# Optimization experiments

Hardware: AMD Instinct MI355X
Metric: run time of the kernel (lower is better)

## Reference

```python
import jax, jax.numpy as jnp
import numpy as np


def setup_inputs() -> dict:
    key = jax.random.key(0)
    k1, k2 = jax.random.split(key)
    B, T, D, K = 16, 800, 256, 64
    x = jax.random.normal(k1, (B, T, D), dtype=jnp.float32)
    mu = jax.random.normal(k2, (K, D), dtype=jnp.float32)
    prec = jnp.ones((K,), dtype=jnp.float32)
    return {"x": x, "mu": mu, "prec": prec}


def reference(x, mu, prec):
    # x: (B,T,D), mu: (K,D), prec: (K,)
    delta = x[:, :, None, :] - mu[None, None, :, :]          # (B,T,K,D)
    dist = jnp.sum(delta * delta, axis=-1)                   # (B,T,K) dist_pow=2
    llk = -(prec * prec) * dist                              # use_bias=False -> bias=0
    r = jax.nn.softmax(llk, axis=-1)                         # softmax over components K
    r = r / (jnp.sum(r, axis=1, keepdims=True) + 1e-9)       # normalize over time T
    pool = jnp.einsum('btk,btkd->bkd', r, delta)             # weighted sum over T
    return pool.reshape(x.shape[0], -1)                      # (B, K*D)
```

## Files before the change

kernel.cpp:

```cpp
#include <hip/hip_runtime.h>

#define B_ 16
#define T_ 800
#define D_ 256
#define K_ 64
#define NTILE 13
#define TSPLIT 8

__global__ __launch_bounds__(512, 1) void kernelA(
    const float* __restrict__ x, const float* __restrict__ mu,
    const float* __restrict__ prec, float* __restrict__ r2, float* __restrict__ Spart)
{
    __shared__ float xs[64 * 260];
    __shared__ float mus[64 * 260];
    __shared__ float xxs[64];
    __shared__ float mms[64];
    __shared__ float sred[8][64];

    const int tid  = threadIdx.x;
    const int tx   = tid >> 4;
    const int ky   = tid & 15;
    const int b    = blockIdx.x / NTILE;
    const int tile = blockIdx.x % NTILE;
    const int t0   = tile * 64;

    #pragma unroll
    for (int jj = 0; jj < 8; ++jj) {
        const int g   = tid + jj * 512;
        const int row = g >> 6, col = g & 63;
        int trow = t0 + row; if (trow > T_ - 1) trow = T_ - 1;
        *(float4*)&xs[row * 260 + col * 4] =
            *(const float4*)(x + ((size_t)(b * T_ + trow)) * D_ + col * 4);
        *(float4*)&mus[row * 260 + col * 4] =
            *(const float4*)(mu + (size_t)row * D_ + col * 4);
    }
    __syncthreads();

    {
        const int srow = tid >> 3, sq = tid & 7;
        float xxp = 0.f, mmp = 0.f;
        #pragma unroll
        for (int m = 0; m < 8; ++m) {
            float4 v = *(const float4*)&xs[srow * 260 + (sq * 8 + m) * 4];
            xxp = fmaf(v.x, v.x, xxp); xxp = fmaf(v.y, v.y, xxp);
            xxp = fmaf(v.z, v.z, xxp); xxp = fmaf(v.w, v.w, xxp);
            float4 u = *(const float4*)&mus[srow * 260 + (sq * 8 + m) * 4];
            mmp = fmaf(u.x, u.x, mmp); mmp = fmaf(u.y, u.y, mmp);
            mmp = fmaf(u.z, u.z, mmp); mmp = fmaf(u.w, u.w, mmp);
        }
        xxp += __shfl_xor(xxp, 1); xxp += __shfl_xor(xxp, 2); xxp += __shfl_xor(xxp, 4);
        mmp += __shfl_xor(mmp, 1); mmp += __shfl_xor(mmp, 2); mmp += __shfl_xor(mmp, 4);
        if (sq == 0) { xxs[srow] = xxp; mms[srow] = mmp; }
    }
    __syncthreads();

    float acc[2][4];
    #pragma unroll
    for (int i = 0; i < 2; ++i)
        #pragma unroll
        for (int j = 0; j < 4; ++j) acc[i][j] = 0.f;

    #pragma unroll 4
    for (int dg = 0; dg < 64; ++dg) {
        float4 xv[2], mv[4];
        #pragma unroll
        for (int i = 0; i < 2; ++i) xv[i] = *(const float4*)&xs[(tx * 2 + i) * 260 + dg * 4];
        #pragma unroll
        for (int j = 0; j < 4; ++j) mv[j] = *(const float4*)&mus[(ky + 16 * j) * 260 + dg * 4];
        #pragma unroll
        for (int i = 0; i < 2; ++i)
            #pragma unroll
            for (int j = 0; j < 4; ++j) {
                float a = acc[i][j];
                a = fmaf(xv[i].x, mv[j].x, a);
                a = fmaf(xv[i].y, mv[j].y, a);
                a = fmaf(xv[i].z, mv[j].z, a);
                a = fmaf(xv[i].w, mv[j].w, a);
                acc[i][j] = a;
            }
    }

    float p2[4], mmk[4];
    #pragma unroll
    for (int j = 0; j < 4; ++j) {
        float p = prec[ky + 16 * j];
        p2[j] = p * p;
        mmk[j] = mms[ky + 16 * j];
    }

    float sacc[4] = {0.f, 0.f, 0.f, 0.f};
    #pragma unroll
    for (int i = 0; i < 2; ++i) {
        const int tl = tx * 2 + i;
        const bool valid = (t0 + tl) < T_;
        const float xxv = xxs[tl];
        float llk[4];
        #pragma unroll
        for (int j = 0; j < 4; ++j)
            llk[j] = p2[j] * (2.f * acc[i][j] - xxv - mmk[j]);
        float mx = fmaxf(fmaxf(llk[0], llk[1]), fmaxf(llk[2], llk[3]));
        mx = fmaxf(mx, __shfl_xor(mx, 1)); mx = fmaxf(mx, __shfl_xor(mx, 2));
        mx = fmaxf(mx, __shfl_xor(mx, 4)); mx = fmaxf(mx, __shfl_xor(mx, 8));
        float e[4], ps = 0.f;
        #pragma unroll
        for (int j = 0; j < 4; ++j) { e[j] = __expf(llk[j] - mx); ps += e[j]; }
        ps += __shfl_xor(ps, 1); ps += __shfl_xor(ps, 2);
        ps += __shfl_xor(ps, 4); ps += __shfl_xor(ps, 8);
        const float inv = 1.f / ps;
        float4 rv;
        rv.x = e[0] * inv; rv.y = e[1] * inv; rv.z = e[2] * inv; rv.w = e[3] * inv;
        if (valid) {
            *(float4*)(r2 + (size_t)(b * T_ + t0 + tl) * K_ + ky * 4) = rv;
            sacc[0] += rv.x; sacc[1] += rv.y; sacc[2] += rv.z; sacc[3] += rv.w;
        }
    }

    #pragma unroll
    for (int j = 0; j < 4; ++j) {
        sacc[j] += __shfl_xor(sacc[j], 16);
        sacc[j] += __shfl_xor(sacc[j], 32);
    }
    const int w = tid >> 6;
    if ((tid & 48) == 0) {
        #pragma unroll
        for (int j = 0; j < 4; ++j) sred[w][ky * 4 + j] = sacc[j];
    }
    __syncthreads();
    if (tid < 64) {
        const int k = tid;
        const int slot = (k & 15) * 4 + (k >> 4);
        float s = 0.f;
        #pragma unroll
        for (int q = 0; q < 8; ++q) s += sred[q][slot];
        Spart[((size_t)b * NTILE + tile) * K_ + k] = s;
    }
}

__global__ __launch_bounds__(256, 2) void kernelB(
    const float* __restrict__ x, const float* __restrict__ r2, float* __restrict__ Pp)
{
    __shared__ float xs[50 * 68];
    __shared__ float rs[50 * 68];

    const int tid = threadIdx.x;
    const int kx  = tid >> 4;
    const int dy  = tid & 15;
    const int bid = blockIdx.x;
    const int b   = bid >> 5;
    const int dc  = (bid >> 3) & 3;
    const int ts  = bid & 7;

    float4 acc[4];
    #pragma unroll
    for (int j = 0; j < 4; ++j) acc[j] = make_float4(0.f, 0.f, 0.f, 0.f);

    #pragma unroll 1
    for (int sc = 0; sc < 2; ++sc) {
        const int tbase = ts * 100 + sc * 50;
        __syncthreads();
        #pragma unroll
        for (int jj = 0; jj < 4; ++jj) {
            const int idx = tid + jj * 256;
            if (idx < 800) {
                const int row = idx >> 4, f4i = idx & 15;
                *(float4*)&xs[row * 68 + f4i * 4] =
                    *(const float4*)(x + (size_t)(b * T_ + tbase + row) * D_ + dc * 64 + f4i * 4);
                *(float4*)&rs[row * 68 + f4i * 4] =
                    *(const float4*)(r2 + (size_t)(b * T_ + tbase + row) * K_ + f4i * 4);
            }
        }
        __syncthreads();
        #pragma unroll 5
        for (int tt = 0; tt < 50; ++tt) {
            const float4 rv = *(const float4*)&rs[tt * 68 + kx * 4];
            const float4 xv = *(const float4*)&xs[tt * 68 + dy * 4];
            acc[0].x = fmaf(rv.x, xv.x, acc[0].x); acc[0].y = fmaf(rv.x, xv.y, acc[0].y);
            acc[0].z = fmaf(rv.x, xv.z, acc[0].z); acc[0].w = fmaf(rv.x, xv.w, acc[0].w);
            acc[1].x = fmaf(rv.y, xv.x, acc[1].x); acc[1].y = fmaf(rv.y, xv.y, acc[1].y);
            acc[1].z = fmaf(rv.y, xv.z, acc[1].z); acc[1].w = fmaf(rv.y, xv.w, acc[1].w);
            acc[2].x = fmaf(rv.z, xv.x, acc[2].x); acc[2].y = fmaf(rv.z, xv.y, acc[2].y);
            acc[2].z = fmaf(rv.z, xv.z, acc[2].z); acc[2].w = fmaf(rv.z, xv.w, acc[2].w);
            acc[3].x = fmaf(rv.w, xv.x, acc[3].x); acc[3].y = fmaf(rv.w, xv.y, acc[3].y);
            acc[3].z = fmaf(rv.w, xv.z, acc[3].z); acc[3].w = fmaf(rv.w, xv.w, acc[3].w);
        }
    }

    #pragma unroll
    for (int j = 0; j < 4; ++j) {
        const int k = kx + 16 * j;
        *(float4*)(Pp + (((size_t)ts * B_ + b) * K_ + k) * D_ + dc * 64 + dy * 4) = acc[j];
    }
}

__global__ __launch_bounds__(256) void kernelC(
    const float* __restrict__ Pp, const float* __restrict__ Spart,
    const float* __restrict__ mu, float* __restrict__ out)
{
    const int o4 = blockIdx.x * 256 + threadIdx.x;
    const int d4 = o4 & 63;
    const int k  = (o4 >> 6) & 63;
    const int b  = o4 >> 12;

    float s = 0.f;
    #pragma unroll
    for (int p = 0; p < NTILE; ++p)
        s += Spart[((size_t)b * NTILE + p) * K_ + k];

    float4 acc = make_float4(0.f, 0.f, 0.f, 0.f);
    #pragma unroll
    for (int ts = 0; ts < TSPLIT; ++ts) {
        float4 v = ((const float4*)Pp)[(((size_t)ts * B_ + b) * K_ + k) * 64 + d4];
        acc.x += v.x; acc.y += v.y; acc.z += v.z; acc.w += v.w;
    }
    const float inv = 1.f / (s + 1e-9f);
    const float sm  = s * inv;
    float4 m = ((const float4*)mu)[k * 64 + d4];
    float4 o;
    o.x = acc.x * inv - sm * m.x;
    o.y = acc.y * inv - sm * m.y;
    o.z = acc.z * inv - sm * m.z;
    o.w = acc.w * inv - sm * m.w;
    ((float4*)out)[o4] = o;
}

extern "C" void kernel_launch(void* const* d_in, const int* in_sizes, int n_in,
                              void* d_out, int out_size, void* d_ws, size_t ws_size,
                              hipStream_t stream) {
    const float* x    = (const float*)d_in[0];
    const float* mu   = (const float*)d_in[1];
    const float* prec = (const float*)d_in[2];
    float* out = (float*)d_out;

    float* r2    = (float*)d_ws;
    float* Pp    = r2 + (size_t)B_ * T_ * K_;
    float* Spart = Pp + (size_t)TSPLIT * B_ * K_ * D_;

    kernelA<<<B_ * NTILE, 512, 0, stream>>>(x, mu, prec, r2, Spart);
    kernelB<<<B_ * 4 * TSPLIT, 256, 0, stream>>>(x, r2, Pp);
    kernelC<<<256, 256, 0, stream>>>(Pp, Spart, mu, out);
}
```

Measured before the change: 88.93 us.

## Fuse responsibility-weighted pooling into distance kernel with atomic accumulation

Merges the softmax kernel and the pooling GEMM kernel into one. Responsibilities are kept in shared memory and multiplied against the x tile already resident in LDS, so the r2 write/read round trip through global memory and one kernel launch go away. Partial pooled sums from the 13 time tiles are combined with float atomicAdd into a zeroed buffer, which replaces the TSPLIT partial buffer and its reduction in kernelC. The cost is a memset, heavy atomic traffic (13 blocks contending per output element), a longer kernelA with extra LDS use, and nondeterministic summation order.

```diff
diff --git a/kernel.cpp b/kernel.cpp
--- a/kernel.cpp
+++ b/kernel.cpp
@@ -5,14 +5,14 @@
 #define D_ 256
 #define K_ 64
 #define NTILE 13
-#define TSPLIT 8
-
-__global__ __launch_bounds__(512, 1) void kernelA(
+
+__global__ __launch_bounds__(512, 1) void kernelAB(
     const float* __restrict__ x, const float* __restrict__ mu,
-    const float* __restrict__ prec, float* __restrict__ r2, float* __restrict__ Spart)
+    const float* __restrict__ prec, float* __restrict__ P, float* __restrict__ Spart)
 {
     __shared__ float xs[64 * 260];
     __shared__ float mus[64 * 260];
+    __shared__ float rt[64 * 68];
     __shared__ float xxs[64];
     __shared__ float mms[64];
     __shared__ float sred[8][64];
@@ -106,13 +106,11 @@
         for (int j = 0; j < 4; ++j) { e[j] = __expf(llk[j] - mx); ps += e[j]; }
         ps += __shfl_xor(ps, 1); ps += __shfl_xor(ps, 2);
         ps += __shfl_xor(ps, 4); ps += __shfl_xor(ps, 8);
-        const float inv = 1.f / ps;
+        const float inv = valid ? (1.f / ps) : 0.f;
         float4 rv;
         rv.x = e[0] * inv; rv.y = e[1] * inv; rv.z = e[2] * inv; rv.w = e[3] * inv;
-        if (valid) {
-            *(float4*)(r2 + (size_t)(b * T_ + t0 + tl) * K_ + ky * 4) = rv;
-            sacc[0] += rv.x; sacc[1] += rv.y; sacc[2] += rv.z; sacc[3] += rv.w;
-        }
+        *(float4*)&rt[tl * 68 + ky * 4] = rv;
+        sacc[0] += rv.x; sacc[1] += rv.y; sacc[2] += rv.z; sacc[3] += rv.w;
     }
 
     #pragma unroll
@@ -134,66 +132,54 @@
         for (int q = 0; q < 8; ++q) s += sred[q][slot];
         Spart[((size_t)b * NTILE + tile) * K_ + k] = s;
     }
+
+    const int dhalf = tid & 31;
+    const int kx2   = tid >> 5;
+
+    float4 pa[4][2];
+    #pragma unroll
+    for (int j = 0; j < 4; ++j) {
+        pa[j][0] = make_float4(0.f, 0.f, 0.f, 0.f);
+        pa[j][1] = make_float4(0.f, 0.f, 0.f, 0.f);
+    }
+
+    #pragma unroll 8
+    for (int tt = 0; tt < 64; ++tt) {
+        const float4 rv  = *(const float4*)&rt[tt * 68 + kx2 * 4];
+        const float4 xv0 = *(const float4*)&xs[tt * 260 + dhalf * 4];
+        const float4 xv1 = *(const float4*)&xs[tt * 260 + 128 + dhalf * 4];
+        #pragma unroll
+        for (int j = 0; j < 4; ++j) {
+            const float rj = (j == 0) ? rv.x : (j == 1) ? rv.y : (j == 2) ? rv.z : rv.w;
+            pa[j][0].x = fmaf(rj, xv0.x, pa[j][0].x);
+            pa[j][0].y = fmaf(rj, xv0.y, pa[j][0].y);
+            pa[j][0].z = fmaf(rj, xv0.z, pa[j][0].z);
+            pa[j][0].w = fmaf(rj, xv0.w, pa[j][0].w);
+            pa[j][1].x = fmaf(rj, xv1.x, pa[j][1].x);
+            pa[j][1].y = fmaf(rj, xv1.y, pa[j][1].y);
+            pa[j][1].z = fmaf(rj, xv1.z, pa[j][1].z);
+            pa[j][1].w = fmaf(rj, xv1.w, pa[j][1].w);
+        }
+    }
+
+    float* Pb = P + (size_t)b * K_ * D_;
+    #pragma unroll
+    for (int j = 0; j < 4; ++j) {
+        const int k = kx2 + 16 * j;
+        float* dst = Pb + (size_t)k * D_ + dhalf * 4;
+        atomicAdd(dst + 0, pa[j][0].x);
+        atomicAdd(dst + 1, pa[j][0].y);
+        atomicAdd(dst + 2, pa[j][0].z);
+        atomicAdd(dst + 3, pa[j][0].w);
+        atomicAdd(dst + 128, pa[j][1].x);
+        atomicAdd(dst + 129, pa[j][1].y);
+        atomicAdd(dst + 130, pa[j][1].z);
+        atomicAdd(dst + 131, pa[j][1].w);
+    }
 }
 
-__global__ __launch_bounds__(256, 2) void kernelB(
-    const float* __restrict__ x, const float* __restrict__ r2, float* __restrict__ Pp)
-{
-    __shared__ float xs[50 * 68];
-    __shared__ float rs[50 * 68];
-
-    const int tid = threadIdx.x;
-    const int kx  = tid >> 4;
-    const int dy  = tid & 15;
-    const int bid = blockIdx.x;
-    const int b   = bid >> 5;
-    const int dc  = (bid >> 3) & 3;
-    const int ts  = bid & 7;
-
-    float4 acc[4];
-    #pragma unroll
-    for (int j = 0; j < 4; ++j) acc[j] = make_float4(0.f, 0.f, 0.f, 0.f);
-
-    #pragma unroll 1
-    for (int sc = 0; sc < 2; ++sc) {
-        const int tbase = ts * 100 + sc * 50;
-        __syncthreads();
-        #pragma unroll
-        for (int jj = 0; jj < 4; ++jj) {
-            const int idx = tid + jj * 256;
-            if (idx < 800) {
-                const int row = idx >> 4, f4i = idx & 15;
-                *(float4*)&xs[row * 68 + f4i * 4] =
-                    *(const float4*)(x + (size_t)(b * T_ + tbase + row) * D_ + dc * 64 + f4i * 4);
-                *(float4*)&rs[row * 68 + f4i * 4] =
-                    *(const float4*)(r2 + (size_t)(b * T_ + tbase + row) * K_ + f4i * 4);
-            }
-        }
-        __syncthreads();
-        #pragma unroll 5
-        for (int tt = 0; tt < 50; ++tt) {
-            const float4 rv = *(const float4*)&rs[tt * 68 + kx * 4];
-            const float4 xv = *(const float4*)&xs[tt * 68 + dy * 4];
-            acc[0].x = fmaf(rv.x, xv.x, acc[0].x); acc[0].y = fmaf(rv.x, xv.y, acc[0].y);
-            acc[0].z = fmaf(rv.x, xv.z, acc[0].z); acc[0].w = fmaf(rv.x, xv.w, acc[0].w);
-            acc[1].x = fmaf(rv.y, xv.x, acc[1].x); acc[1].y = fmaf(rv.y, xv.y, acc[1].y);
-            acc[1].z = fmaf(rv.y, xv.z, acc[1].z); acc[1].w = fmaf(rv.y, xv.w, acc[1].w);
-            acc[2].x = fmaf(rv.z, xv.x, acc[2].x); acc[2].y = fmaf(rv.z, xv.y, acc[2].y);
-            acc[2].z = fmaf(rv.z, xv.z, acc[2].z); acc[2].w = fmaf(rv.z, xv.w, acc[2].w);
-            acc[3].x = fmaf(rv.w, xv.x, acc[3].x); acc[3].y = fmaf(rv.w, xv.y, acc[3].y);
-            acc[3].z = fmaf(rv.w, xv.z, acc[3].z); acc[3].w = fmaf(rv.w, xv.w, acc[3].w);
-        }
-    }
-
-    #pragma unroll
-    for (int j = 0; j < 4; ++j) {
-        const int k = kx + 16 * j;
-        *(float4*)(Pp + (((size_t)ts * B_ + b) * K_ + k) * D_ + dc * 64 + dy * 4) = acc[j];
-    }
-}
-
 __global__ __launch_bounds__(256) void kernelC(
-    const float* __restrict__ Pp, const float* __restrict__ Spart,
+    const float* __restrict__ P, const float* __restrict__ Spart,
     const float* __restrict__ mu, float* __restrict__ out)
 {
     const int o4 = blockIdx.x * 256 + threadIdx.x;
@@ -206,20 +192,15 @@
     for (int p = 0; p < NTILE; ++p)
         s += Spart[((size_t)b * NTILE + p) * K_ + k];
 
-    float4 acc = make_float4(0.f, 0.f, 0.f, 0.f);
-    #pragma unroll
-    for (int ts = 0; ts < TSPLIT; ++ts) {
-        float4 v = ((const float4*)Pp)[(((size_t)ts * B_ + b) * K_ + k) * 64 + d4];
-        acc.x += v.x; acc.y += v.y; acc.z += v.z; acc.w += v.w;
-    }
+    const float4 pv = ((const float4*)P)[o4];
     const float inv = 1.f / (s + 1e-9f);
     const float sm  = s * inv;
-    float4 m = ((const float4*)mu)[k * 64 + d4];
+    const float4 m = ((const float4*)mu)[k * 64 + d4];
     float4 o;
-    o.x = acc.x * inv - sm * m.x;
-    o.y = acc.y * inv - sm * m.y;
-    o.z = acc.z * inv - sm * m.z;
-    o.w = acc.w * inv - sm * m.w;
+    o.x = pv.x * inv - sm * m.x;
+    o.y = pv.y * inv - sm * m.y;
+    o.z = pv.z * inv - sm * m.z;
+    o.w = pv.w * inv - sm * m.w;
     ((float4*)out)[o4] = o;
 }
 
@@ -231,11 +212,10 @@
     const float* prec = (const float*)d_in[2];
     float* out = (float*)d_out;
 
-    float* r2    = (float*)d_ws;
-    float* Pp    = r2 + (size_t)B_ * T_ * K_;
-    float* Spart = Pp + (size_t)TSPLIT * B_ * K_ * D_;
-
-    kernelA<<<B_ * NTILE, 512, 0, stream>>>(x, mu, prec, r2, Spart);
-    kernelB<<<B_ * 4 * TSPLIT, 256, 0, stream>>>(x, r2, Pp);
-    kernelC<<<256, 256, 0, stream>>>(Pp, Spart, mu, out);
+    float* P     = (float*)d_ws;
+    float* Spart = P + (size_t)B_ * K_ * D_;
+
+    hipMemsetAsync(P, 0, (size_t)B_ * K_ * D_ * sizeof(float), stream);
+    kernelAB<<<B_ * NTILE, 512, 0, stream>>>(x, mu, prec, P, Spart);
+    kernelC<<<256, 256, 0, stream>>>(P, Spart, mu, out);
 }
```

Result: slower. 153.4 us (+72.5%).
